# Performance work log

Measured on AMD Instinct MI355X. Metric: run time of the kernel, lower is better.

## Reference

```python
import jax, jax.numpy as jnp
import numpy as np

NEG_SLOPE = 0.2
EPS = 1e-8
N, E, IN_F, OUT_F, H = 50000, 800000, 256, 32, 8


def setup_inputs() -> dict:
    key = jax.random.key(0)
    k1, k2, k3, k4, k5 = jax.random.split(key, 5)
    x = jax.random.normal(k1, (N, IN_F), dtype=jnp.float32)
    edge_index = jax.random.randint(k2, (2, E), 0, N, dtype=jnp.int32)
    # xavier_uniform bounds as in torch reset_parameters
    bw = float(np.sqrt(6.0 / (IN_F + OUT_F)))
    W = jax.random.uniform(k3, (H, IN_F, OUT_F), minval=-bw, maxval=bw, dtype=jnp.float32)
    ba = float(np.sqrt(6.0 / (OUT_F + 1)))
    a_src = jax.random.uniform(k4, (H, OUT_F), minval=-ba, maxval=ba, dtype=jnp.float32)
    a_dst = jax.random.uniform(k5, (H, OUT_F), minval=-ba, maxval=ba, dtype=jnp.float32)
    return {"x": x, "edge_index": edge_index, "W": W, "a_src": a_src, "a_dst": a_dst}


def reference(x, edge_index, W, a_src, a_dst):
    num_nodes = x.shape[0]
    src, dst = edge_index[0], edge_index[1]
    # per-head linear transform: [H, N, F]
    h = jnp.einsum('ni,hif->hnf', x, W)
    # per-node attention logits (a_src/a_dst are the squeezed [H,F] vectors)
    s_src = jnp.einsum('hnf,hf->hn', h, a_src)  # [H, N]
    s_dst = jnp.einsum('hnf,hf->hn', h, a_dst)  # [H, N]
    # edge scores + LeakyReLU, laid out [E, H] for segment ops
    ea = (s_src[:, src] + s_dst[:, dst]).T  # [E, H]
    ea = jnp.where(ea > 0, ea, NEG_SLOPE * ea)
    # sparse softmax over incoming edges of each destination node
    m = jax.ops.segment_max(ea, dst, num_segments=num_nodes)  # [N, H]
    ea = jnp.exp(ea - m[dst])
    s = jax.ops.segment_sum(ea, dst, num_segments=num_nodes)  # [N, H]
    ea = ea / (s[dst] + EPS)  # [E, H]
    # weighted scatter-add aggregation (dropout is identity in eval)
    hn = jnp.transpose(h, (1, 0, 2))  # [N, H, F]
    wf = hn[src] * ea[:, :, None]  # [E, H, F]
    out = jax.ops.segment_sum(wf, dst, num_segments=num_nodes)  # [N, H, F]
    # concat heads -> [N, H*F]
    return out.reshape(num_nodes, -1)
```

## Files before the change

kernel.cpp:

```cpp
#include <hip/hip_runtime.h>
#include <stdint.h>

#define NN 50000
#define EE 800000
#define INF_ 256
#define OUTF 32
#define HH 8
#define NEG_SLOPE 0.2f
#define EPS_ 1e-8f
#define NPART 8
#define CAPX 16

typedef unsigned short u16;
typedef unsigned int u32;
typedef short bf16x8 __attribute__((ext_vector_type(8)));
typedef float f32x4 __attribute__((ext_vector_type(4)));

__device__ __forceinline__ float bflo(u32 w){ return __uint_as_float(w << 16); }
__device__ __forceinline__ float bfhi(u32 w){ return __uint_as_float(w & 0xFFFF0000u); }
__device__ __forceinline__ u16 f2bf(float f){
  u32 u = __float_as_uint(f);
  u += 0x7FFFu + ((u >> 16) & 1u);
  return (u16)(u >> 16);
}

#define PREP_B 272

__global__ void k_prep(const float* __restrict__ W, const float* __restrict__ a_src,
                       const float* __restrict__ a_dst, u16* __restrict__ Wt,
                       int* __restrict__ cnt){
  int t = threadIdx.x;
  for (int z = blockIdx.x*256 + t; z < NPART*NN; z += PREP_B*256) cnt[z] = 0;
  if (t >= 64) return;
  int n = blockIdx.x;
  int k4 = t * 4;
  ushort4 o;
  if (n < 256){
    int h = n >> 5, f = n & 31;
    const float* Wh = W + h*(INF_*OUTF) + f;
    o.x = f2bf(Wh[(k4+0)*OUTF]);
    o.y = f2bf(Wh[(k4+1)*OUTF]);
    o.z = f2bf(Wh[(k4+2)*OUTF]);
    o.w = f2bf(Wh[(k4+3)*OUTF]);
  } else {
    int j = n - 256;
    int h = j >> 1;
    const float* av = (j & 1) ? (a_dst + h*OUTF) : (a_src + h*OUTF);
    const float* Wh = W + h*(INF_*OUTF);
    float r[4];
#pragma unroll
    for (int i=0;i<4;i++){
      const float4* Wk = (const float4*)(Wh + (k4+i)*OUTF);
      const float4* A4 = (const float4*)av;
      float s = 0.f;
#pragma unroll
      for (int q=0;q<8;q++){
        float4 w = Wk[q], a = A4[q];
        s += w.x*a.x + w.y*a.y + w.z*a.z + w.w*a.w;
      }
      r[i] = s;
    }
    o.x=f2bf(r[0]); o.y=f2bf(r[1]); o.z=f2bf(r[2]); o.w=f2bf(r[3]);
  }
  *(ushort4*)(Wt + n*INF_ + k4) = o;
}

#define BM 64
#define BK 32
#define NB 272
#define LDA 56
#define GEMM_B 782
#define APP_B  3125

__global__ __launch_bounds__(256, 2) void k_ga(const float* __restrict__ x,
    const u16* __restrict__ Wt, u16* __restrict__ h_out,
    float* __restrict__ s_src, float* __restrict__ s_dst,
    const int* __restrict__ ei, int* __restrict__ cnt, u16* __restrict__ slots){
  __shared__ __align__(16) u16 As[BM*LDA];
  __shared__ __align__(16) u16 Bs[NB*LDA];
  int tid = threadIdx.x;

  if (blockIdx.x >= GEMM_B){
    int ab = blockIdx.x - GEMM_B;
    int e = ab*256 + tid;
    if (e < EE){
      int d = ei[EE + e];
      int p = ab & (NPART-1);
      int pos = atomicAdd(&cnt[p*NN + d], 1);
      if (pos < CAPX) slots[(p*NN + d)*CAPX + pos] = (u16)ei[e];
    }
    return;
  }

  int n0 = blockIdx.x * BM;
  int wv = tid >> 6, lane = tid & 63;
  int lr = lane & 15, lg = lane >> 4;

  f32x4 zero4 = {0.f,0.f,0.f,0.f};
  f32x4 acc[4][4];
  f32x4 acc2[4];
#pragma unroll
  for (int m=0;m<4;m++){
    acc2[m] = zero4;
#pragma unroll
    for (int n=0;n<4;n++) acc[m][n] = zero4;
  }

  int a_row = tid >> 3;
  int a_c4  = tid & 7;
  u32 a_off = (u32)a_row*LDA + (a_c4&3)*8 + (a_c4>>2)*4;

  float4 a_reg[2];
  uint4  b_reg[5];

#pragma unroll
  for (int i=0;i<2;i++){
    int n = n0 + a_row + i*32;
    a_reg[i] = (n < NN) ? *(const float4*)(x + n*INF_ + a_c4*4)
                        : make_float4(0.f,0.f,0.f,0.f);
  }
#pragma unroll
  for (int i=0;i<5;i++){
    int idx = tid + i*256;
    if (idx < NB*4){
      int col = idx >> 2, c16 = idx & 3;
      b_reg[i] = *(const uint4*)(Wt + col*INF_ + c16*8);
    }
  }

  for (int step = 0; step < 8; ++step){
    __syncthreads();
#pragma unroll
    for (int i=0;i<2;i++){
      float4 u = a_reg[i];
      ushort4 o; o.x=f2bf(u.x); o.y=f2bf(u.y); o.z=f2bf(u.z); o.w=f2bf(u.w);
      *(ushort4*)(As + a_off + i*32*LDA) = o;
    }
#pragma unroll
    for (int i=0;i<5;i++){
      int idx = tid + i*256;
      if (idx < NB*4){
        int col = idx >> 2, c16 = idx & 3;
        u32 off = (u32)col*LDA + (c16&1)*16 + (c16>>1)*4;
        uint4 b = b_reg[i];
        *(uint2*)(Bs + off)     = make_uint2(b.x, b.y);
        *(uint2*)(Bs + off + 8) = make_uint2(b.z, b.w);
      }
    }
    __syncthreads();
    if (step < 7){
      int k0 = (step+1)*BK;
#pragma unroll
      for (int i=0;i<2;i++){
        int n = n0 + a_row + i*32;
        a_reg[i] = (n < NN) ? *(const float4*)(x + n*INF_ + k0 + a_c4*4)
                            : make_float4(0.f,0.f,0.f,0.f);
      }
#pragma unroll
      for (int i=0;i<5;i++){
        int idx = tid + i*256;
        if (idx < NB*4){
          int col = idx >> 2, c16 = idx & 3;
          b_reg[i] = *(const uint4*)(Wt + col*INF_ + k0 + c16*8);
        }
      }
    }
    bf16x8 af[4];
#pragma unroll
    for (int m=0;m<4;m++)
      af[m] = *(const bf16x8*)(As + (m*16+lr)*LDA + lg*8);
    int cb = wv*64;
#pragma unroll
    for (int n=0;n<4;n++){
      bf16x8 bv = *(const bf16x8*)(Bs + (cb + n*16 + lr)*LDA + lg*8);
#pragma unroll
      for (int m=0;m<4;m++)
        acc[m][n] = __builtin_amdgcn_mfma_f32_16x16x32_bf16(af[m], bv, acc[m][n], 0, 0, 0);
    }
    if (wv == 0){
      bf16x8 b2 = *(const bf16x8*)(Bs + (256 + lr)*LDA + lg*8);
#pragma unroll
      for (int m=0;m<4;m++)
        acc2[m] = __builtin_amdgcn_mfma_f32_16x16x32_bf16(af[m], b2, acc2[m], 0, 0, 0);
    }
  }

#pragma unroll
  for (int m=0;m<4;m++){
#pragma unroll
    for (int r=0;r<4;r++){
      int row = m*16 + lg*4 + r;
      int n = n0 + row;
      if (n >= NN) continue;
      u16* dst = h_out + n*INF_ + wv*64 + lr;
      dst[0]  = f2bf(acc[m][0][r]);
      dst[16] = f2bf(acc[m][1][r]);
      dst[32] = f2bf(acc[m][2][r]);
      dst[48] = f2bf(acc[m][3][r]);
    }
  }
  if (wv == 0){
    int h = lr >> 1;
    float* sp = (lr & 1) ? s_dst : s_src;
#pragma unroll
    for (int m=0;m<4;m++){
#pragma unroll
      for (int r=0;r<4;r++){
        int n = n0 + m*16 + lg*4 + r;
        if (n < NN) sp[n*8 + h] = acc2[m][r];
      }
    }
  }
}

__global__ __launch_bounds__(256) void k_agg(const int* __restrict__ cnt,
    const u16* __restrict__ slots, const float* __restrict__ s_src,
    const float* __restrict__ s_dst, const u16* __restrict__ h_bf,
    float* __restrict__ out){
  int lane = threadIdx.x & 63;
  int n = blockIdx.x*4 + (threadIdx.x >> 6);
  if (n >= NN) return;
  int eh = lane >> 5;
  int hh = (lane >> 2) & 7;
  int q4 = lane & 3;
  int pfx[NPART]; int d = 0;
#pragma unroll
  for (int p=0;p<NPART;p++){
    pfx[p] = d;
    int cc = cnt[p*NN + n];
    d += (cc > CAPX) ? CAPX : cc;
  }
  int my_src = 0;
  if (lane < d){
    int p = 0;
#pragma unroll
    for (int q=1;q<NPART;q++) if (lane >= pfx[q]) p = q;
    my_src = (int)slots[(p*NN + n)*CAPX + (lane - pfx[p])];
  }
  float sd = s_dst[n*8 + hh];
  const u16* hb = h_bf + hh*32 + q4*8;
  float l = 0.f;
  float a[8];
#pragma unroll
  for (int k=0;k<8;k++) a[k] = 0.f;
  for (int e0 = 0; e0 < d; e0 += 8){
    int se[4]; float vs[4]; uint4 v[4];
#pragma unroll
    for (int i=0;i<4;i++) se[i] = __shfl(my_src, e0 + 2*i + eh, 64);
#pragma unroll
    for (int i=0;i<4;i++) v[i] = *(const uint4*)(hb + se[i]*INF_);
#pragma unroll
    for (int i=0;i<4;i++) vs[i] = s_src[se[i]*8 + hh];
#pragma unroll
    for (int i=0;i<4;i++){
      float sc = vs[i] + sd;
      sc = fmaxf(sc, NEG_SLOPE*sc);
      float p = (e0 + 2*i + eh < d) ? __expf(sc) : 0.f;
      l += p;
      a[0] += p*bflo(v[i].x); a[1] += p*bfhi(v[i].x);
      a[2] += p*bflo(v[i].y); a[3] += p*bfhi(v[i].y);
      a[4] += p*bflo(v[i].z); a[5] += p*bfhi(v[i].z);
      a[6] += p*bflo(v[i].w); a[7] += p*bfhi(v[i].w);
    }
  }
  l += __shfl_xor(l, 32, 64);
#pragma unroll
  for (int k=0;k<8;k++) a[k] += __shfl_xor(a[k], 32, 64);
  float inv = 1.f/(l + EPS_);
  float4 o = make_float4(a[eh*4+0]*inv, a[eh*4+1]*inv,
                         a[eh*4+2]*inv, a[eh*4+3]*inv);
  *(float4*)(out + n*INF_ + hh*32 + q4*8 + eh*4) = o;
}

extern "C" void kernel_launch(void* const* d_in, const int* in_sizes, int n_in,
                              void* d_out, int out_size, void* d_ws, size_t ws_size,
                              hipStream_t stream){
  const float* x     = (const float*)d_in[0];
  const int*   ei    = (const int*)d_in[1];
  const float* W     = (const float*)d_in[2];
  const float* a_src = (const float*)d_in[3];
  const float* a_dst = (const float*)d_in[4];
  float* out = (float*)d_out;
  char* ws = (char*)d_ws;

  u16*   h_bf    = (u16*)  (ws + 0);
  float* s_src   = (float*)(ws + 25600000);
  float* s_dst   = (float*)(ws + 27200000);
  int*   cnt     = (int*)  (ws + 28800000);
  u16*   slots   = (u16*)  (ws + 30400000);
  u16*   Wt      = (u16*)  (ws + 43200000);

  k_prep<<<PREP_B, 256, 0, stream>>>(W, a_src, a_dst, Wt, cnt);
  k_ga<<<GEMM_B + APP_B, 256, 0, stream>>>(x, Wt, h_bf, s_src, s_dst, ei, cnt, slots);
  k_agg<<<(NN + 3)/4, 256, 0, stream>>>(cnt, slots, s_src, s_dst, h_bf, out);
}
```

Before: 216.5 us.

## Double-buffer aggregation gathers and batch two edges per bucketing thread

The aggregation loop becomes a two-stage software pipeline: the gathers of the next 8 source rows are issued before the current 8 are computed, so memory latency overlaps with the exp and FMA work. The bucketing blocks now each handle two edges per thread, halving the number of append blocks, and the GEMM kernel's launch bounds rise to 4 blocks per SM. The degree is also clamped to 64, which the shuffle already implied. Costs are more registers in k_agg, and possible spills in the GEMM path under the tighter launch bound.

```diff
diff --git a/kernel.cpp b/kernel.cpp
--- a/kernel.cpp
+++ b/kernel.cpp
@@ -70,9 +70,9 @@
 #define NB 272
 #define LDA 56
 #define GEMM_B 782
-#define APP_B  3125
-
-__global__ __launch_bounds__(256, 2) void k_ga(const float* __restrict__ x,
+#define APP_B  1563
+
+__global__ __launch_bounds__(256, 4) void k_ga(const float* __restrict__ x,
     const u16* __restrict__ Wt, u16* __restrict__ h_out,
     float* __restrict__ s_src, float* __restrict__ s_dst,
     const int* __restrict__ ei, int* __restrict__ cnt, u16* __restrict__ slots){
@@ -82,13 +82,18 @@
 
   if (blockIdx.x >= GEMM_B){
     int ab = blockIdx.x - GEMM_B;
-    int e = ab*256 + tid;
-    if (e < EE){
-      int d = ei[EE + e];
-      int p = ab & (NPART-1);
-      int pos = atomicAdd(&cnt[p*NN + d], 1);
-      if (pos < CAPX) slots[(p*NN + d)*CAPX + pos] = (u16)ei[e];
-    }
+    int p = ab & (NPART-1);
+    int e0 = ab*512 + tid;
+    int e1 = e0 + 256;
+    bool b1 = e1 < EE;
+    int d0 = ei[EE + e0];
+    int d1 = b1 ? ei[EE + e1] : 0;
+    int s0 = ei[e0];
+    int s1 = b1 ? ei[e1] : 0;
+    int pos0 = atomicAdd(&cnt[p*NN + d0], 1);
+    int pos1 = b1 ? atomicAdd(&cnt[p*NN + d1], 1) : CAPX;
+    if (pos0 < CAPX) slots[(p*NN + d0)*CAPX + pos0] = (u16)s0;
+    if (pos1 < CAPX) slots[(p*NN + d1)*CAPX + pos1] = (u16)s1;
     return;
   }
 
@@ -212,6 +217,28 @@
     }
   }
 }
+
+#define AGG_LOAD(SE, V, VS, BASE) do{                                     \
+  _Pragma("unroll") for (int i=0;i<4;i++)                                 \
+    SE[i] = __shfl(my_src, (BASE) + 2*i + eh, 64);                        \
+  _Pragma("unroll") for (int i=0;i<4;i++)                                 \
+    V[i] = *(const uint4*)(hb + SE[i]*INF_);                              \
+  _Pragma("unroll") for (int i=0;i<4;i++)                                 \
+    VS[i] = s_src[SE[i]*8 + hh];                                          \
+}while(0)
+
+#define AGG_COMP(V, VS, BASE) do{                                         \
+  _Pragma("unroll") for (int i=0;i<4;i++){                                \
+    float sc = VS[i] + sd;                                                \
+    sc = fmaxf(sc, NEG_SLOPE*sc);                                         \
+    float p = ((BASE) + 2*i + eh < d) ? __expf(sc) : 0.f;                 \
+    l += p;                                                               \
+    a[0] += p*bflo(V[i].x); a[1] += p*bfhi(V[i].x);                       \
+    a[2] += p*bflo(V[i].y); a[3] += p*bfhi(V[i].y);                       \
+    a[4] += p*bflo(V[i].z); a[5] += p*bfhi(V[i].z);                       \
+    a[6] += p*bflo(V[i].w); a[7] += p*bfhi(V[i].w);                       \
+  }                                                                       \
+}while(0)
 
 __global__ __launch_bounds__(256) void k_agg(const int* __restrict__ cnt,
     const u16* __restrict__ slots, const float* __restrict__ s_src,
@@ -230,6 +257,7 @@
     int cc = cnt[p*NN + n];
     d += (cc > CAPX) ? CAPX : cc;
   }
+  if (d > 64) d = 64;
   int my_src = 0;
   if (lane < d){
     int p = 0;
@@ -243,24 +271,20 @@
   float a[8];
 #pragma unroll
   for (int k=0;k<8;k++) a[k] = 0.f;
-  for (int e0 = 0; e0 < d; e0 += 8){
-    int se[4]; float vs[4]; uint4 v[4];
-#pragma unroll
-    for (int i=0;i<4;i++) se[i] = __shfl(my_src, e0 + 2*i + eh, 64);
-#pragma unroll
-    for (int i=0;i<4;i++) v[i] = *(const uint4*)(hb + se[i]*INF_);
-#pragma unroll
-    for (int i=0;i<4;i++) vs[i] = s_src[se[i]*8 + hh];
-#pragma unroll
-    for (int i=0;i<4;i++){
-      float sc = vs[i] + sd;
-      sc = fmaxf(sc, NEG_SLOPE*sc);
-      float p = (e0 + 2*i + eh < d) ? __expf(sc) : 0.f;
-      l += p;
-      a[0] += p*bflo(v[i].x); a[1] += p*bfhi(v[i].x);
-      a[2] += p*bflo(v[i].y); a[3] += p*bfhi(v[i].y);
-      a[4] += p*bflo(v[i].z); a[5] += p*bfhi(v[i].z);
-      a[6] += p*bflo(v[i].w); a[7] += p*bfhi(v[i].w);
+
+  if (d > 0){
+    int seA[4], seB[4]; float vsA[4], vsB[4]; uint4 vA[4], vB[4];
+    AGG_LOAD(seA, vA, vsA, 0);
+    int e0 = 0;
+    for (;;){
+      if (e0 + 8 < d) AGG_LOAD(seB, vB, vsB, e0 + 8);
+      AGG_COMP(vA, vsA, e0);
+      e0 += 8;
+      if (e0 >= d) break;
+      if (e0 + 8 < d) AGG_LOAD(seA, vA, vsA, e0 + 8);
+      AGG_COMP(vB, vsB, e0);
+      e0 += 8;
+      if (e0 >= d) break;
     }
   }
   l += __shfl_xor(l, 32, 64);
```

Result: slower. 242.5 us (+12.0%).
